# Kernel optimization log

Hardware: AMD Instinct MI355X
Metric: run time of the kernel (lower is better)

The kernel has to match this reference:

```python
import jax, jax.numpy as jnp
import numpy as np

N_ATOMS = 4096
N_NEIGH = 32
IN_F = 128
HID = 256
OUT_F = 128
N_SPECIES = 64


def setup_inputs() -> dict:
    key = jax.random.key(0)
    k1, k2, k3, k4, k5, k6 = jax.random.split(key, 6)
    # kaiming-uniform-ish init scales (exact init doesn't matter for correctness testing)
    s1 = 1.0 / np.sqrt(IN_F)
    s2 = 1.0 / np.sqrt(HID)
    return {
        "features": jax.random.normal(k1, (N_ATOMS, N_NEIGH, IN_F), dtype=jnp.float32),
        "species_idx": jax.random.randint(k2, (N_ATOMS,), 0, N_SPECIES, dtype=jnp.int64 if jax.config.jax_enable_x64 else jnp.int32),
        "W1": jax.random.uniform(k3, (N_SPECIES, HID, IN_F), jnp.float32, -s1, s1),
        "b1": jax.random.uniform(k4, (N_SPECIES, HID), jnp.float32, -s1, s1),
        "W2": jax.random.uniform(k5, (N_SPECIES, OUT_F, HID), jnp.float32, -s2, s2),
        "b2": jax.random.uniform(k6, (N_SPECIES, OUT_F), jnp.float32, -s2, s2),
    }


def reference(features, species_idx, W1, b1, W2, b2):
    # Per-atom species-conditioned 2-layer MLP with SiLU after the hidden layer.
    # features: (A, N, in); W[idx]: (A, out, in) gathered per atom (as in torch W[idx]).
    x = jnp.einsum("ani,ahi->anh", features, W1[species_idx]) + b1[species_idx][:, None, :]
    x = jax.nn.silu(x)
    x = jnp.einsum("anh,aoh->ano", x, W2[species_idx]) + b2[species_idx][:, None, :]
    return x  # (A, N, out)
```

## Files before the change

kernel.cpp:

```cpp
#include <hip/hip_runtime.h>

typedef __attribute__((ext_vector_type(8))) short short8;
typedef __attribute__((ext_vector_type(4))) float f32x4;

#define N_ATOMS 4096
#define N_NEIGH 32
#define IN_F 128
#define HID 256
#define OUT_F 128
#define N_SPECIES 64
#define GRP 8
#define MAX_GROUPS 576

__device__ __forceinline__ unsigned short f2bf(float f) {
  unsigned u = __float_as_uint(f);
  u += 0x7FFF + ((u >> 16) & 1);
  return (unsigned short)(u >> 16);
}
struct HL { short h, l; };
__device__ __forceinline__ HL split2(float v) {
  unsigned u = __float_as_uint(v);
  float lo = v - __uint_as_float(u & 0xFFFF0000u);
  HL o;
  o.h = (short)(u >> 16);
  o.l = (short)(__float_as_uint(lo) >> 16);
  return o;
}

__global__ __launch_bounds__(256) void prep_kernel(
    const float* __restrict__ W1, const float* __restrict__ W2,
    const int* __restrict__ sp_idx,
    unsigned short* __restrict__ w1h, unsigned short* __restrict__ w2h,
    int* __restrict__ atom_order, int* __restrict__ grp_sp,
    int* __restrict__ grp_base, int* __restrict__ grp_cnt,
    int* __restrict__ n_groups) {
  const int t = threadIdx.x;
  if (blockIdx.x == 0) {
    __shared__ int cnt[N_SPECIES], off[N_SPECIES], cur[N_SPECIES], gb[N_SPECIES];
    if (t < N_SPECIES) cnt[t] = 0;
    __syncthreads();
    for (int a = t; a < N_ATOMS; a += 256) atomicAdd(&cnt[sp_idx[a]], 1);
    __syncthreads();
    if (t == 0) {
      int o = 0, g = 0;
      for (int s = 0; s < N_SPECIES; ++s) {
        off[s] = o; cur[s] = o; gb[s] = g;
        o += cnt[s];
        g += (cnt[s] + GRP - 1) / GRP;
      }
      *n_groups = g;
    }
    __syncthreads();
    for (int a = t; a < N_ATOMS; a += 256) {
      int s = sp_idx[a];
      atom_order[atomicAdd(&cur[s], 1)] = a;
    }
    if (t < N_SPECIES) {
      const int c = cnt[t], base = off[t], g0 = gb[t];
      const int ng = (c + GRP - 1) / GRP;
      for (int j = 0; j < ng; ++j) {
        grp_sp[g0 + j]   = t;
        grp_base[g0 + j] = base + j * GRP;
        grp_cnt[g0 + j]  = min(GRP, c - j * GRP);
      }
    }
    return;
  }
  const int NV = (N_SPECIES * HID * IN_F) / 4;
  const int nsplit = (gridDim.x - 1) * 256;
  for (int v = (blockIdx.x - 1) * 256 + t; v < 2 * NV; v += nsplit) {
    const float4* src; unsigned short* dh; int j;
    if (v < NV) { src = (const float4*)W1; dh = w1h; j = v; }
    else        { src = (const float4*)W2; dh = w2h; j = v - NV; }
    float4 f = src[j];
    ushort4 h;
    h.x = f2bf(f.x); h.y = f2bf(f.y); h.z = f2bf(f.z); h.w = f2bf(f.w);
    ((ushort4*)dh)[j] = h;
  }
}

__global__ __launch_bounds__(512, 2) void mlp_kernel(
    const float* __restrict__ feat,
    const float* __restrict__ b1g, const float* __restrict__ b2g,
    const unsigned short* __restrict__ w1h, const unsigned short* __restrict__ w2h,
    const int* __restrict__ atom_order, const int* __restrict__ grp_sp,
    const int* __restrict__ grp_base, const int* __restrict__ grp_cnt,
    const int* __restrict__ n_groups,
    float* __restrict__ out) {
  extern __shared__ char smem[];
  char* LW1 = smem;
  char* LW2 = smem + 65536;

  const int bid = blockIdx.x;
  const int g = (bid & 7) * (MAX_GROUPS / 8) + (bid >> 3);
  if (g >= *n_groups) return;
  const int s = grp_sp[g];
  const int abase = grp_base[g];
  const int cnt = grp_cnt[g];
  const int tid = threadIdx.x;
  const int wave = tid >> 6, lane = tid & 63;
  const int q = lane >> 4, r = lane & 15;
  const bool active = (wave < cnt);

  {
    const char* gw1 = (const char*)w1h + (long)s * (HID * IN_F * 2);
    const char* gw2 = (const char*)w2h + (long)s * (OUT_F * HID * 2);
#pragma unroll
    for (int it = 0; it < 8; ++it) {
      const int d = it * 8192 + tid * 16;
      const int h = d >> 8, w = d & 255;
      const int src = h * (IN_F * 2) + (w ^ ((h & 7) << 4));
      __builtin_amdgcn_global_load_lds(
          (const __attribute__((address_space(1))) unsigned int*)(gw1 + src),
          (__attribute__((address_space(3))) unsigned int*)(LW1 + d), 16, 0, 0);
    }
#pragma unroll
    for (int it = 0; it < 8; ++it) {
      const int d = it * 8192 + tid * 16;
      const int o = d >> 9, w = d & 511;
      const int src = o * (HID * 2) + (w ^ ((o & 7) << 4));
      __builtin_amdgcn_global_load_lds(
          (const __attribute__((address_space(1))) unsigned int*)(gw2 + src),
          (__attribute__((address_space(3))) unsigned int*)(LW2 + d), 16, 0, 0);
    }
  }

  short8 fh[2][4], fl[2][4];
  int atom = 0;
  if (active) {
    atom = atom_order[abase + wave];
    const float* fb = feat + (long)atom * (N_NEIGH * IN_F);
#pragma unroll
    for (int nt = 0; nt < 2; ++nt)
#pragma unroll
      for (int ks = 0; ks < 4; ++ks) {
        const float* p = fb + (16 * nt + r) * IN_F + 32 * ks + 8 * q;
        float4 v0 = *(const float4*)p;
        float4 v1 = *(const float4*)(p + 4);
        float vv[8] = {v0.x, v0.y, v0.z, v0.w, v1.x, v1.y, v1.z, v1.w};
        short8 h8, l8;
#pragma unroll
        for (int j = 0; j < 8; ++j) {
          HL hl = split2(vv[j]);
          h8[j] = hl.h;
          l8[j] = hl.l;
        }
        fh[nt][ks] = h8;
        fl[nt][ks] = l8;
      }
  }

  asm volatile("s_waitcnt vmcnt(0)" ::: "memory");
  __syncthreads();

  if (!active) return;

  f32x4 oacc[2][8] = {};
  char* lxw = smem + 131072 + wave * 4096;
  const int swz = (r & 7) << 4;
  const float* b1s = b1g + s * HID;

  for (int hc = 0; hc < 8; ++hc) {
    f32x4 xacc[2][2] = {};
#pragma unroll
    for (int ks = 0; ks < 4; ++ks) {
      const int ib = ((32 * ks + 8 * q) * 2) ^ swz;
#pragma unroll
      for (int ht = 0; ht < 2; ++ht) {
        const int row = 32 * hc + 16 * ht + r;
        short8 bh = *(const short8*)(LW1 + row * 256 + ib);
        xacc[0][ht] = __builtin_amdgcn_mfma_f32_16x16x32_bf16(fh[0][ks], bh, xacc[0][ht], 0, 0, 0);
        xacc[1][ht] = __builtin_amdgcn_mfma_f32_16x16x32_bf16(fh[1][ks], bh, xacc[1][ht], 0, 0, 0);
        xacc[0][ht] = __builtin_amdgcn_mfma_f32_16x16x32_bf16(fl[0][ks], bh, xacc[0][ht], 0, 0, 0);
        xacc[1][ht] = __builtin_amdgcn_mfma_f32_16x16x32_bf16(fl[1][ks], bh, xacc[1][ht], 0, 0, 0);
      }
    }
#pragma unroll
    for (int ht = 0; ht < 2; ++ht) {
      const float b1v = b1s[hc * 32 + 16 * ht + r];
#pragma unroll
      for (int nt = 0; nt < 2; ++nt)
#pragma unroll
        for (int i = 0; i < 4; ++i) {
          const int n = 16 * nt + 4 * q + i;
          float v = xacc[nt][ht][i] + b1v;
          v = v * __builtin_amdgcn_rcpf(1.0f + __expf(-v));
          const int byte = n * 128 + (((16 * ht + r) * 4) ^ ((q & 1) << 6));
          *(float*)(lxw + byte) = v;
        }
    }
    short8 ah[2], al[2];
#pragma unroll
    for (int nt = 0; nt < 2; ++nt) {
      const int n = 16 * nt + r;
      const int base_b = n * 128 + ((32 * q) ^ (((r >> 2) & 1) << 6));
      float4 v0 = *(const float4*)(lxw + base_b);
      float4 v1 = *(const float4*)(lxw + base_b + 16);
      float vv[8] = {v0.x, v0.y, v0.z, v0.w, v1.x, v1.y, v1.z, v1.w};
      short8 h8, l8;
#pragma unroll
      for (int j = 0; j < 8; ++j) {
        HL hl = split2(vv[j]);
        h8[j] = hl.h;
        l8[j] = hl.l;
      }
      ah[nt] = h8;
      al[nt] = l8;
    }
    const int kb = ((32 * hc + 8 * q) * 2) ^ swz;
#pragma unroll
    for (int ot = 0; ot < 8; ++ot) {
      const int row = 16 * ot + r;
      short8 bw = *(const short8*)(LW2 + row * 512 + kb);
      oacc[0][ot] = __builtin_amdgcn_mfma_f32_16x16x32_bf16(ah[0], bw, oacc[0][ot], 0, 0, 0);
      oacc[1][ot] = __builtin_amdgcn_mfma_f32_16x16x32_bf16(ah[1], bw, oacc[1][ot], 0, 0, 0);
      oacc[0][ot] = __builtin_amdgcn_mfma_f32_16x16x32_bf16(al[0], bw, oacc[0][ot], 0, 0, 0);
      oacc[1][ot] = __builtin_amdgcn_mfma_f32_16x16x32_bf16(al[1], bw, oacc[1][ot], 0, 0, 0);
    }
  }

  float* ob = out + (long)atom * (N_NEIGH * OUT_F);
#pragma unroll
  for (int ot = 0; ot < 8; ++ot) {
    const float b2v = b2g[s * OUT_F + 16 * ot + r];
#pragma unroll
    for (int nt = 0; nt < 2; ++nt)
#pragma unroll
      for (int i = 0; i < 4; ++i) {
        ob[(16 * nt + 4 * q + i) * OUT_F + 16 * ot + r] = oacc[nt][ot][i] + b2v;
      }
  }
}

extern "C" void kernel_launch(void* const* d_in, const int* in_sizes, int n_in,
                              void* d_out, int out_size, void* d_ws, size_t ws_size,
                              hipStream_t stream) {
  const float* feat = (const float*)d_in[0];
  const int* sp     = (const int*)d_in[1];
  const float* W1   = (const float*)d_in[2];
  const float* b1   = (const float*)d_in[3];
  const float* W2   = (const float*)d_in[4];
  const float* b2   = (const float*)d_in[5];
  float* out = (float*)d_out;

  char* ws = (char*)d_ws;
  unsigned short* w1h = (unsigned short*)(ws + 0);
  unsigned short* w2h = (unsigned short*)(ws + 4194304);
  int* atom_order = (int*)(ws + 8388608);
  int* grp_sp     = (int*)(ws + 8388608 + 16384);
  int* grp_base   = (int*)(ws + 8388608 + 16384 + 4352);
  int* grp_cnt    = (int*)(ws + 8388608 + 16384 + 8704);
  int* n_groups   = (int*)(ws + 8388608 + 16384 + 13056);

  hipFuncSetAttribute((const void*)mlp_kernel,
                      hipFuncAttributeMaxDynamicSharedMemorySize, 163840);

  hipLaunchKernelGGL(prep_kernel, dim3(1025), dim3(256), 0, stream,
                     W1, W2, sp, w1h, w2h,
                     atom_order, grp_sp, grp_base, grp_cnt, n_groups);
  hipLaunchKernelGGL(mlp_kernel, dim3(MAX_GROUPS), dim3(512), 163840, stream,
                     feat, b1, b2, w1h, w2h,
                     atom_order, grp_sp, grp_base, grp_cnt, n_groups, out);
}
```

Before: 192.2 us.

## Use persistent per-species blocks looping over atoms with prefetched features

Replaces the grid of up to 576 blocks of 8 atoms each with 256 blocks, four per species. Each block loads that species' bf16 weights into LDS once, and its waves loop over the block's share of atoms. While the current atom is computed, the next atom's features are prefetched into registers. This cuts repeated weight staging into LDS and the idle waves in partial groups. The costs are higher register pressure from the 16-float4 prefetch buffer and load imbalance when species counts are uneven. The LDS swizzle for the hidden activations is also changed.

```diff
diff --git a/kernel.cpp b/kernel.cpp
--- a/kernel.cpp
+++ b/kernel.cpp
@@ -9,8 +9,6 @@
 #define HID 256
 #define OUT_F 128
 #define N_SPECIES 64
-#define GRP 8
-#define MAX_GROUPS 576
 
 __device__ __forceinline__ unsigned short f2bf(float f) {
   unsigned u = __float_as_uint(f);
@@ -31,39 +29,24 @@
     const float* __restrict__ W1, const float* __restrict__ W2,
     const int* __restrict__ sp_idx,
     unsigned short* __restrict__ w1h, unsigned short* __restrict__ w2h,
-    int* __restrict__ atom_order, int* __restrict__ grp_sp,
-    int* __restrict__ grp_base, int* __restrict__ grp_cnt,
-    int* __restrict__ n_groups) {
+    int* __restrict__ atom_order, int* __restrict__ sp_off, int* __restrict__ sp_cnt) {
   const int t = threadIdx.x;
   if (blockIdx.x == 0) {
-    __shared__ int cnt[N_SPECIES], off[N_SPECIES], cur[N_SPECIES], gb[N_SPECIES];
+    __shared__ int cnt[N_SPECIES], off[N_SPECIES], cur[N_SPECIES];
     if (t < N_SPECIES) cnt[t] = 0;
     __syncthreads();
     for (int a = t; a < N_ATOMS; a += 256) atomicAdd(&cnt[sp_idx[a]], 1);
     __syncthreads();
     if (t == 0) {
-      int o = 0, g = 0;
-      for (int s = 0; s < N_SPECIES; ++s) {
-        off[s] = o; cur[s] = o; gb[s] = g;
-        o += cnt[s];
-        g += (cnt[s] + GRP - 1) / GRP;
-      }
-      *n_groups = g;
+      int o = 0;
+      for (int s = 0; s < N_SPECIES; ++s) { off[s] = o; cur[s] = o; o += cnt[s]; }
     }
     __syncthreads();
     for (int a = t; a < N_ATOMS; a += 256) {
       int s = sp_idx[a];
       atom_order[atomicAdd(&cur[s], 1)] = a;
     }
-    if (t < N_SPECIES) {
-      const int c = cnt[t], base = off[t], g0 = gb[t];
-      const int ng = (c + GRP - 1) / GRP;
-      for (int j = 0; j < ng; ++j) {
-        grp_sp[g0 + j]   = t;
-        grp_base[g0 + j] = base + j * GRP;
-        grp_cnt[g0 + j]  = min(GRP, c - j * GRP);
-      }
-    }
+    if (t < N_SPECIES) { sp_off[t] = off[t]; sp_cnt[t] = cnt[t]; }
     return;
   }
   const int NV = (N_SPECIES * HID * IN_F) / 4;
@@ -83,24 +66,19 @@
     const float* __restrict__ feat,
     const float* __restrict__ b1g, const float* __restrict__ b2g,
     const unsigned short* __restrict__ w1h, const unsigned short* __restrict__ w2h,
-    const int* __restrict__ atom_order, const int* __restrict__ grp_sp,
-    const int* __restrict__ grp_base, const int* __restrict__ grp_cnt,
-    const int* __restrict__ n_groups,
+    const int* __restrict__ atom_order, const int* __restrict__ sp_off,
+    const int* __restrict__ sp_cnt,
     float* __restrict__ out) {
   extern __shared__ char smem[];
   char* LW1 = smem;
   char* LW2 = smem + 65536;
 
   const int bid = blockIdx.x;
-  const int g = (bid & 7) * (MAX_GROUPS / 8) + (bid >> 3);
-  if (g >= *n_groups) return;
-  const int s = grp_sp[g];
-  const int abase = grp_base[g];
-  const int cnt = grp_cnt[g];
+  const int s = (bid & 7) * 8 + (bid >> 5);
+  const int p = (bid >> 3) & 3;
   const int tid = threadIdx.x;
   const int wave = tid >> 6, lane = tid & 63;
   const int q = lane >> 4, r = lane & 15;
-  const bool active = (wave < cnt);
 
   {
     const char* gw1 = (const char*)w1h + (long)s * (HID * IN_F * 2);
@@ -125,18 +103,46 @@
     }
   }
 
-  short8 fh[2][4], fl[2][4];
-  int atom = 0;
-  if (active) {
-    atom = atom_order[abase + wave];
+  const int c = sp_cnt[s], base = sp_off[s];
+  const int begin = base + (p * c) / 4;
+  const int end   = base + ((p + 1) * c) / 4;
+
+  float b2v[8];
+#pragma unroll
+  for (int ot = 0; ot < 8; ++ot) b2v[ot] = b2g[s * OUT_F + 16 * ot + r];
+  const float* b1s = b1g + s * HID;
+
+  char* lxw = smem + 131072 + wave * 4096;
+  const int swz = (r & 7) << 4;
+
+  float4 R[16];
+  auto ISSUE = [&](int atom) {
     const float* fb = feat + (long)atom * (N_NEIGH * IN_F);
 #pragma unroll
     for (int nt = 0; nt < 2; ++nt)
 #pragma unroll
       for (int ks = 0; ks < 4; ++ks) {
-        const float* p = fb + (16 * nt + r) * IN_F + 32 * ks + 8 * q;
-        float4 v0 = *(const float4*)p;
-        float4 v1 = *(const float4*)(p + 4);
+        const float* ptr = fb + (16 * nt + r) * IN_F + 32 * ks + 8 * q;
+        R[nt * 8 + ks * 2]     = *(const float4*)ptr;
+        R[nt * 8 + ks * 2 + 1] = *(const float4*)(ptr + 4);
+      }
+  };
+
+  int idx = begin + wave;
+  int a_cur = 0;
+  if (idx < end) { a_cur = atom_order[idx]; ISSUE(a_cur); }
+
+  asm volatile("s_waitcnt vmcnt(0)" ::: "memory");
+  __syncthreads();
+
+  while (idx < end) {
+    short8 fh[2][4], fl[2][4];
+#pragma unroll
+    for (int nt = 0; nt < 2; ++nt)
+#pragma unroll
+      for (int ks = 0; ks < 4; ++ks) {
+        float4 v0 = R[nt * 8 + ks * 2];
+        float4 v1 = R[nt * 8 + ks * 2 + 1];
         float vv[8] = {v0.x, v0.y, v0.z, v0.w, v1.x, v1.y, v1.z, v1.w};
         short8 h8, l8;
 #pragma unroll
@@ -148,87 +154,80 @@
         fh[nt][ks] = h8;
         fl[nt][ks] = l8;
       }
-  }
-
-  asm volatile("s_waitcnt vmcnt(0)" ::: "memory");
-  __syncthreads();
-
-  if (!active) return;
-
-  f32x4 oacc[2][8] = {};
-  char* lxw = smem + 131072 + wave * 4096;
-  const int swz = (r & 7) << 4;
-  const float* b1s = b1g + s * HID;
-
-  for (int hc = 0; hc < 8; ++hc) {
-    f32x4 xacc[2][2] = {};
-#pragma unroll
-    for (int ks = 0; ks < 4; ++ks) {
-      const int ib = ((32 * ks + 8 * q) * 2) ^ swz;
+    const int atom_here = a_cur;
+    const int nidx = idx + 8;
+    if (nidx < end) { a_cur = atom_order[nidx]; ISSUE(a_cur); }
+
+    f32x4 oacc[2][8] = {};
+    for (int hc = 0; hc < 8; ++hc) {
+      f32x4 xacc[2][2] = {};
+#pragma unroll
+      for (int ks = 0; ks < 4; ++ks) {
+        const int ib = ((32 * ks + 8 * q) * 2) ^ swz;
+#pragma unroll
+        for (int ht = 0; ht < 2; ++ht) {
+          const int row = 32 * hc + 16 * ht + r;
+          short8 bh = *(const short8*)(LW1 + row * 256 + ib);
+          xacc[0][ht] = __builtin_amdgcn_mfma_f32_16x16x32_bf16(fh[0][ks], bh, xacc[0][ht], 0, 0, 0);
+          xacc[1][ht] = __builtin_amdgcn_mfma_f32_16x16x32_bf16(fh[1][ks], bh, xacc[1][ht], 0, 0, 0);
+          xacc[0][ht] = __builtin_amdgcn_mfma_f32_16x16x32_bf16(fl[0][ks], bh, xacc[0][ht], 0, 0, 0);
+          xacc[1][ht] = __builtin_amdgcn_mfma_f32_16x16x32_bf16(fl[1][ks], bh, xacc[1][ht], 0, 0, 0);
+        }
+      }
 #pragma unroll
       for (int ht = 0; ht < 2; ++ht) {
-        const int row = 32 * hc + 16 * ht + r;
-        short8 bh = *(const short8*)(LW1 + row * 256 + ib);
-        xacc[0][ht] = __builtin_amdgcn_mfma_f32_16x16x32_bf16(fh[0][ks], bh, xacc[0][ht], 0, 0, 0);
-        xacc[1][ht] = __builtin_amdgcn_mfma_f32_16x16x32_bf16(fh[1][ks], bh, xacc[1][ht], 0, 0, 0);
-        xacc[0][ht] = __builtin_amdgcn_mfma_f32_16x16x32_bf16(fl[0][ks], bh, xacc[0][ht], 0, 0, 0);
-        xacc[1][ht] = __builtin_amdgcn_mfma_f32_16x16x32_bf16(fl[1][ks], bh, xacc[1][ht], 0, 0, 0);
-      }
-    }
-#pragma unroll
-    for (int ht = 0; ht < 2; ++ht) {
-      const float b1v = b1s[hc * 32 + 16 * ht + r];
+        const float b1v = b1s[hc * 32 + 16 * ht + r];
+#pragma unroll
+        for (int nt = 0; nt < 2; ++nt)
+#pragma unroll
+          for (int i = 0; i < 4; ++i) {
+            const int n = 16 * nt + 4 * q + i;
+            float v = xacc[nt][ht][i] + b1v;
+            v = v * __builtin_amdgcn_rcpf(1.0f + __expf(-v));
+            const int byte = n * 128 + (((16 * ht + r) * 4) ^ ((n & 7) << 4));
+            *(float*)(lxw + byte) = v;
+          }
+      }
+      short8 ah[2], al[2];
+#pragma unroll
+      for (int nt = 0; nt < 2; ++nt) {
+        const int n = 16 * nt + r;
+        float4 v0 = *(const float4*)(lxw + n * 128 + ((32 * q) ^ swz));
+        float4 v1 = *(const float4*)(lxw + n * 128 + ((32 * q + 16) ^ swz));
+        float vv[8] = {v0.x, v0.y, v0.z, v0.w, v1.x, v1.y, v1.z, v1.w};
+        short8 h8, l8;
+#pragma unroll
+        for (int j = 0; j < 8; ++j) {
+          HL hl = split2(vv[j]);
+          h8[j] = hl.h;
+          l8[j] = hl.l;
+        }
+        ah[nt] = h8;
+        al[nt] = l8;
+      }
+      const int kb = ((32 * hc + 8 * q) * 2) ^ swz;
+#pragma unroll
+      for (int ot = 0; ot < 8; ++ot) {
+        const int row = 16 * ot + r;
+        short8 bw = *(const short8*)(LW2 + row * 512 + kb);
+        oacc[0][ot] = __builtin_amdgcn_mfma_f32_16x16x32_bf16(ah[0], bw, oacc[0][ot], 0, 0, 0);
+        oacc[1][ot] = __builtin_amdgcn_mfma_f32_16x16x32_bf16(ah[1], bw, oacc[1][ot], 0, 0, 0);
+        oacc[0][ot] = __builtin_amdgcn_mfma_f32_16x16x32_bf16(al[0], bw, oacc[0][ot], 0, 0, 0);
+        oacc[1][ot] = __builtin_amdgcn_mfma_f32_16x16x32_bf16(al[1], bw, oacc[1][ot], 0, 0, 0);
+      }
+    }
+
+    float* ob = out + (long)atom_here * (N_NEIGH * OUT_F);
+#pragma unroll
+    for (int ot = 0; ot < 8; ++ot)
 #pragma unroll
       for (int nt = 0; nt < 2; ++nt)
 #pragma unroll
         for (int i = 0; i < 4; ++i) {
-          const int n = 16 * nt + 4 * q + i;
-          float v = xacc[nt][ht][i] + b1v;
-          v = v * __builtin_amdgcn_rcpf(1.0f + __expf(-v));
-          const int byte = n * 128 + (((16 * ht + r) * 4) ^ ((q & 1) << 6));
-          *(float*)(lxw + byte) = v;
-        }
-    }
-    short8 ah[2], al[2];
-#pragma unroll
-    for (int nt = 0; nt < 2; ++nt) {
-      const int n = 16 * nt + r;
-      const int base_b = n * 128 + ((32 * q) ^ (((r >> 2) & 1) << 6));
-      float4 v0 = *(const float4*)(lxw + base_b);
-      float4 v1 = *(const float4*)(lxw + base_b + 16);
-      float vv[8] = {v0.x, v0.y, v0.z, v0.w, v1.x, v1.y, v1.z, v1.w};
-      short8 h8, l8;
-#pragma unroll
-      for (int j = 0; j < 8; ++j) {
-        HL hl = split2(vv[j]);
-        h8[j] = hl.h;
-        l8[j] = hl.l;
-      }
-      ah[nt] = h8;
-      al[nt] = l8;
-    }
-    const int kb = ((32 * hc + 8 * q) * 2) ^ swz;
-#pragma unroll
-    for (int ot = 0; ot < 8; ++ot) {
-      const int row = 16 * ot + r;
-      short8 bw = *(const short8*)(LW2 + row * 512 + kb);
-      oacc[0][ot] = __builtin_amdgcn_mfma_f32_16x16x32_bf16(ah[0], bw, oacc[0][ot], 0, 0, 0);
-      oacc[1][ot] = __builtin_amdgcn_mfma_f32_16x16x32_bf16(ah[1], bw, oacc[1][ot], 0, 0, 0);
-      oacc[0][ot] = __builtin_amdgcn_mfma_f32_16x16x32_bf16(al[0], bw, oacc[0][ot], 0, 0, 0);
-      oacc[1][ot] = __builtin_amdgcn_mfma_f32_16x16x32_bf16(al[1], bw, oacc[1][ot], 0, 0, 0);
-    }
-  }
-
-  float* ob = out + (long)atom * (N_NEIGH * OUT_F);
-#pragma unroll
-  for (int ot = 0; ot < 8; ++ot) {
-    const float b2v = b2g[s * OUT_F + 16 * ot + r];
-#pragma unroll
-    for (int nt = 0; nt < 2; ++nt)
-#pragma unroll
-      for (int i = 0; i < 4; ++i) {
-        ob[(16 * nt + 4 * q + i) * OUT_F + 16 * ot + r] = oacc[nt][ot][i] + b2v;
-      }
+          ob[(16 * nt + 4 * q + i) * OUT_F + 16 * ot + r] = oacc[nt][ot][i] + b2v[ot];
+        }
+
+    idx = nidx;
   }
 }
 
@@ -247,18 +246,14 @@
   unsigned short* w1h = (unsigned short*)(ws + 0);
   unsigned short* w2h = (unsigned short*)(ws + 4194304);
   int* atom_order = (int*)(ws + 8388608);
-  int* grp_sp     = (int*)(ws + 8388608 + 16384);
-  int* grp_base   = (int*)(ws + 8388608 + 16384 + 4352);
-  int* grp_cnt    = (int*)(ws + 8388608 + 16384 + 8704);
-  int* n_groups   = (int*)(ws + 8388608 + 16384 + 13056);
+  int* sp_off     = (int*)(ws + 8388608 + 16384);
+  int* sp_cnt     = (int*)(ws + 8388608 + 16384 + 256);
 
   hipFuncSetAttribute((const void*)mlp_kernel,
                       hipFuncAttributeMaxDynamicSharedMemorySize, 163840);
 
   hipLaunchKernelGGL(prep_kernel, dim3(1025), dim3(256), 0, stream,
-                     W1, W2, sp, w1h, w2h,
-                     atom_order, grp_sp, grp_base, grp_cnt, n_groups);
-  hipLaunchKernelGGL(mlp_kernel, dim3(MAX_GROUPS), dim3(512), 163840, stream,
-                     feat, b1, b2, w1h, w2h,
-                     atom_order, grp_sp, grp_base, grp_cnt, n_groups, out);
-}
+                     W1, W2, sp, w1h, w2h, atom_order, sp_off, sp_cnt);
+  hipLaunchKernelGGL(mlp_kernel, dim3(256), dim3(512), 163840, stream,
+                     feat, b1, b2, w1h, w2h, atom_order, sp_off, sp_cnt, out);
+}
```

New measurement: 198.0 us. +3.0%, slower.
